# Optimization experiments

Measured on AMD Instinct MI355X. Metric: run time of the kernel, lower is better.

Reference implementation:

```python
import jax, jax.numpy as jnp
import numpy as np

B, IN, O, F, FH = 512, 2000, 64, 8, 32
D = 64 + FH * O  # 2112


def setup_inputs() -> dict:
    key = jax.random.key(0)
    ks = jax.random.split(key, 17)
    rn = lambda k, s: jax.random.normal(k, s, dtype=jnp.float32) * 0.05
    return dict(
        x=rn(ks[0], (B, IN)),
        fc_in_W=rn(ks[1], (1024, IN)), fc_in_b=rn(ks[2], (1024,)),
        fc1_W=rn(ks[3], (128, 1024)), fc1_b=rn(ks[4], (128,)),
        out1_W=rn(ks[5], (O, 64, 128)), out1_b=rn(ks[6], (O, 64)),
        coef_nn_W=rn(ks[7], (F, FH, 1)), coef_nn_b=rn(ks[8], (F, FH)),
        coef_att_W=rn(ks[9], (F, FH, FH)),
        out_att_W=rn(ks[10], (O, FH, FH)),
        nodes_trans_W=rn(ks[11], (O, O)),
        trans_gcn_W=rn(ks[12], (D, D)),
        outmap_W=rn(ks[13], (1, D)), outmap_b=rn(ks[14], (1,)),
        prelu_a=jnp.float32(0.25),
        coef_m=rn(ks[15], (O, O, F)),
    )


def reference(x, fc_in_W, fc_in_b, fc1_W, fc1_b, out1_W, out1_b,
              coef_nn_W, coef_nn_b, coef_att_W, out_att_W,
              nodes_trans_W, trans_gcn_W, outmap_W, outmap_b, prelu_a, coef_m):
    elu = jax.nn.elu
    # trunk MLP
    h = jax.nn.relu(x @ fc_in_W.T + fc_in_b)          # [B,1024]
    h = jax.nn.relu(h @ fc1_W.T + fc1_b)              # [B,128]
    # per-output-node heads (vectorized over the output_dim loop)
    hiddens = jax.nn.relu(jnp.einsum('bk,odk->bod', h, out1_W) + out1_b)  # [B,O,64]
    # per-feature coef embedding: Linear(1,FH) on each coef_m[:,:,i] slice
    cf = elu(coef_m[..., None] * coef_nn_W[:, :, 0] + coef_nn_b)          # [O,O,F,FH]
    # sum over concatenated feature axis (F*FH) of exp(elu(.))
    s = jnp.exp(elu(cf)).sum(axis=(2, 3))[:, :, None, None]               # [O,O,1,1]
    lin = jnp.einsum('xyfh,fgh->xyfg', cf, coef_att_W)                    # per-feature attention linear
    p = elu(jnp.exp(elu(cf)) * lin / s)
    cfs = elu(p.sum(axis=2) / F)                                          # [O,O,FH]
    # node-level attention (vectorized over the output_dim loop)
    coef_sum = jnp.exp(elu(cfs)).sum(axis=1)                              # [O,FH]
    p2 = jnp.exp(elu(cfs)) / coef_sum[:, None, :]                         # [O,O,FH]
    lin2 = jnp.einsum('oih,igh->oig', cfs, out_att_W)
    att = (p2 * lin2).reshape(O, O * FH)                                  # concat over i (i-major)
    hc = jnp.concatenate(
        [hiddens, jnp.broadcast_to(att[None], (x.shape[0], O, O * FH))], axis=2)  # [B,O,D]
    nt = jnp.einsum('bpd,op->bod', hc, nodes_trans_W)                     # node mixing Linear(O,O)
    trans = jax.nn.sigmoid(jnp.einsum('bod,ed->boe', nt, trans_gcn_W))    # [B,O,D]
    z = (trans @ outmap_W.T + outmap_b).squeeze(-1)                       # [B,O]
    return jnp.where(z >= 0, z, prelu_a * z)                              # PReLU
```

## Files before the change

### kernel.cpp

```cpp
#include <hip/hip_runtime.h>
#include <math.h>

typedef __attribute__((ext_vector_type(8))) short bf16x8;
typedef __attribute__((ext_vector_type(4))) float f32x4;

static __device__ __forceinline__ float fast_elu(float x) {
    return x > 0.0f ? x : __expf(x) - 1.0f;
}

static __device__ __forceinline__ unsigned short f2bf(float f) {
    unsigned int u = __float_as_uint(f);
    unsigned int r = (u + 0x7FFFu + ((u >> 16) & 1u)) >> 16;
    return (unsigned short)r;
}

static __device__ __forceinline__ bf16x8 cvt8(const float* __restrict__ s) {
    float4 a = *reinterpret_cast<const float4*>(s);
    float4 b = *reinterpret_cast<const float4*>(s + 4);
    bf16x8 r;
    r[0] = (short)f2bf(a.x); r[1] = (short)f2bf(a.y);
    r[2] = (short)f2bf(a.z); r[3] = (short)f2bf(a.w);
    r[4] = (short)f2bf(b.x); r[5] = (short)f2bf(b.y);
    r[6] = (short)f2bf(b.z); r[7] = (short)f2bf(b.w);
    return r;
}

#define S0 131072
#define S1 393216
#define S2 409600
#define S3 410112
#define S4 475648
#define S5 492544
#define CONV_BLOCKS 1924

static __device__ __forceinline__ void conv_phase(
    int bx,
    const float* __restrict__ x, const float* __restrict__ fcinW,
    const float* __restrict__ fc1W, const float* __restrict__ ntW,
    const float* __restrict__ out1W, const float* __restrict__ tgw,
    unsigned short* __restrict__ xb, unsigned short* __restrict__ fcinWb,
    unsigned short* __restrict__ fc1Wb, unsigned short* __restrict__ Wb,
    unsigned short* __restrict__ out1WbT, unsigned short* __restrict__ Gb)
{
    int u = bx * 256 + threadIdx.x;
    if (u < S0) {
        int r = u >> 8, c = u & 255;
        bf16x8 v;
        if (c < 250) v = cvt8(&x[(size_t)r * 2000 + c * 8]);
        else { bf16x8 z = {0,0,0,0,0,0,0,0}; v = z; }
        *reinterpret_cast<bf16x8*>(&xb[(size_t)r * 2048 + c * 8]) = v;
    } else if (u < S1) {
        int i = u - S0;
        int r = i >> 8, c = i & 255;
        bf16x8 v;
        if (c < 250) v = cvt8(&fcinW[(size_t)r * 2000 + c * 8]);
        else { bf16x8 z = {0,0,0,0,0,0,0,0}; v = z; }
        *reinterpret_cast<bf16x8*>(&fcinWb[(size_t)r * 2048 + c * 8]) = v;
    } else if (u < S2) {
        int i8 = (u - S1) * 8;
        *reinterpret_cast<bf16x8*>(&fc1Wb[i8]) = cvt8(&fc1W[i8]);
    } else if (u < S3) {
        int i8 = (u - S2) * 8;
        *reinterpret_cast<bf16x8*>(&Wb[i8]) = cvt8(&ntW[i8]);
    } else if (u < S4) {
        int i = u - S3;
        int n = i >> 4, kc = i & 15;
        int d = n >> 6, p = n & 63;
        *reinterpret_cast<bf16x8*>(&out1WbT[(size_t)n * 128 + kc * 8]) =
            cvt8(&out1W[(size_t)((p << 6) | d) * 128 + kc * 8]);
    } else if (u < S5) {
        int i = u - S4;
        int e = i >> 3, c = i & 7;
        *reinterpret_cast<bf16x8*>(&Gb[(size_t)e * 64 + c * 8]) =
            cvt8(&tgw[(size_t)e * 2112 + c * 8]);
    }
}

static __device__ __forceinline__ void coef_phase(
    int bx, float* __restrict__ smemf,
    const float* __restrict__ coef_m, const float* __restrict__ cW,
    const float* __restrict__ cB, const float* __restrict__ attW,
    float* __restrict__ cfs)
{
    float* cf_s = smemf;
    float* part = smemf + 1024;
    const int t = threadIdx.x;
    const int wv = t >> 6, lane = t & 63;
    const int xy = bx * 4 + wv;
    float ls = 0.0f;
    #pragma unroll
    for (int i = 0; i < 4; ++i) {
        int idx = i * 64 + lane;
        int f = idx >> 5;
        float v = fast_elu(coef_m[xy * 8 + f] * cW[idx] + cB[idx]);
        cf_s[wv * 256 + idx] = v;
        ls += __expf(fast_elu(v));
    }
    #pragma unroll
    for (int m = 1; m < 64; m <<= 1) ls += __shfl_xor(ls, m, 64);
    __syncthreads();
    const float rs = __builtin_amdgcn_rcpf(ls);
    const int g = lane & 31, fg = lane >> 5;
    float acc = 0.0f;
    for (int f = fg * 4; f < fg * 4 + 4; ++f) {
        float lin = 0.0f;
        #pragma unroll
        for (int h = 0; h < 32; h += 4) {
            float4 Lv = *reinterpret_cast<const float4*>(&cf_s[wv * 256 + f * 32 + h]);
            float4 Wv = *reinterpret_cast<const float4*>(&attW[f * 1024 + g * 32 + h]);
            lin += Lv.x * Wv.x + Lv.y * Wv.y + Lv.z * Wv.z + Lv.w * Wv.w;
        }
        float e = __expf(fast_elu(cf_s[wv * 256 + f * 32 + g]));
        acc += fast_elu(e * lin * rs);
    }
    part[wv * 64 + lane] = acc;
    __syncthreads();
    if (lane < 32) {
        float tot = part[wv * 64 + lane] + part[wv * 64 + lane + 32];
        cfs[xy * 32 + lane] = fast_elu(tot * 0.125f);
    }
}

static __device__ __forceinline__ void att_phase(
    int o, int ic, float* __restrict__ smemf,
    const float* __restrict__ cfs, const float* __restrict__ oattW,
    float* __restrict__ att)
{
    float* L    = smemf;
    float* red  = smemf + 2048;
    float* csum = smemf + 2304;
    const int t = threadIdx.x;
    #pragma unroll
    for (int j = 0; j < 8; ++j) L[t + 256 * j] = cfs[o * 2048 + t + 256 * j];
    __syncthreads();
    {
        int h = t & 31, ig = t >> 5;
        float ps = 0.0f;
        for (int i = ig * 8; i < ig * 8 + 8; ++i) ps += __expf(fast_elu(L[i * 32 + h]));
        red[t] = ps;
        __syncthreads();
        if (t < 32) {
            float cs = 0.0f;
            #pragma unroll
            for (int j = 0; j < 8; ++j) cs += red[j * 32 + t];
            csum[t] = cs;
        }
        __syncthreads();
    }
    int idx = ic * 256 + t;
    int i = idx >> 5, g = idx & 31;
    float lin2 = 0.0f;
    #pragma unroll
    for (int h = 0; h < 32; h += 4) {
        float4 Lv = *reinterpret_cast<const float4*>(&L[i * 32 + h]);
        float4 Wv = *reinterpret_cast<const float4*>(&oattW[i * 1024 + g * 32 + h]);
        lin2 += Lv.x * Wv.x + Lv.y * Wv.y + Lv.z * Wv.z + Lv.w * Wv.w;
    }
    float p2 = __expf(fast_elu(L[idx])) * __builtin_amdgcn_rcpf(csum[g]);
    att[o * 2048 + idx] = p2 * lin2;
}

static __device__ __forceinline__ void natt_phase(
    int bx, float* __restrict__ smemf,
    const float* __restrict__ ntW, const float* __restrict__ att,
    unsigned short* __restrict__ nattb)
{
    float* ntW_s = smemf;
    float* att_s = smemf + 64 * 65;
    const int t = threadIdx.x;
    const int d0 = bx * 16;
    #pragma unroll
    for (int j = 0; j < 16; ++j) {
        int idx = t + 256 * j;
        ntW_s[(idx >> 6) * 65 + (idx & 63)] = ntW[idx];
    }
    #pragma unroll
    for (int j = 0; j < 4; ++j) {
        int idx = t + 256 * j;
        int p = idx >> 4, dd = idx & 15;
        att_s[p * 17 + dd] = att[p * 2048 + d0 + dd];
    }
    __syncthreads();
    const int dd = t & 15, ob = (t >> 4) * 4;
    float acc[4] = {0.0f, 0.0f, 0.0f, 0.0f};
    for (int p = 0; p < 64; ++p) {
        float av = att_s[p * 17 + dd];
        #pragma unroll
        for (int i = 0; i < 4; ++i) acc[i] += ntW_s[(ob + i) * 65 + p] * av;
    }
    #pragma unroll
    for (int i = 0; i < 4; ++i)
        nattb[(ob + i) * 2048 + d0 + dd] = f2bf(acc[i]);
}

static __device__ __forceinline__ void gemm_core(
    const unsigned short* __restrict__ A, int lda,
    const unsigned short* __restrict__ B, int ldb,
    float* __restrict__ C, unsigned short* __restrict__ Cb,
    int ldc, long strideCz, const float* __restrict__ bias,
    int mode, int kchunk, int bn, int bm, int bz,
    unsigned short* __restrict__ As, unsigned short* __restrict__ Bs)
{
    const int t = threadIdx.x;
    const int w = t >> 6, lane = t & 63, l16 = lane & 15, quad = lane >> 4;
    const int n0 = bn * 64, m0 = bm * 64;
    const int kb0 = bz * kchunk;
    const int r = t >> 2, koff = (t & 3) * 8;
    if (mode == 0) C += (size_t)bz * strideCz;

    const size_t arow = (size_t)(m0 + r) * lda + koff;
    const size_t brow = (size_t)(n0 + r) * ldb + koff;
    bf16x8 av = *reinterpret_cast<const bf16x8*>(&A[arow + kb0]);
    bf16x8 bv = *reinterpret_cast<const bf16x8*>(&B[brow + kb0]);

    f32x4 acc[4] = {};
    for (int kb = kb0; kb < kb0 + kchunk; kb += 32) {
        __syncthreads();
        *reinterpret_cast<bf16x8*>(&As[r * 40 + koff]) = av;
        *reinterpret_cast<bf16x8*>(&Bs[r * 40 + koff]) = bv;
        if (kb + 32 < kb0 + kchunk) {
            av = *reinterpret_cast<const bf16x8*>(&A[arow + kb + 32]);
            bv = *reinterpret_cast<const bf16x8*>(&B[brow + kb + 32]);
        }
        __syncthreads();
        bf16x8 af = *reinterpret_cast<const bf16x8*>(&As[(w * 16 + l16) * 40 + quad * 8]);
        #pragma unroll
        for (int nt = 0; nt < 4; ++nt) {
            bf16x8 bf = *reinterpret_cast<const bf16x8*>(&Bs[(nt * 16 + l16) * 40 + quad * 8]);
            acc[nt] = __builtin_amdgcn_mfma_f32_16x16x32_bf16(af, bf, acc[nt], 0, 0, 0);
        }
    }
    #pragma unroll
    for (int nt = 0; nt < 4; ++nt)
        #pragma unroll
        for (int i = 0; i < 4; ++i) {
            int m = m0 + w * 16 + quad * 4 + i;
            int n = n0 + nt * 16 + l16;
            if (mode == 0) {
                C[(size_t)m * ldc + n] = acc[nt][i];
            } else {
                int bidx = (((n & 63) << 6) | (n >> 6));
                float v = acc[nt][i] + bias[bidx];
                v = fmaxf(v, 0.0f);
                Cb[(size_t)m * ldc + n] = f2bf(v);
            }
        }
}

static __device__ __forceinline__ void gemm_tgwa_core(
    const float* __restrict__ tgw,
    const unsigned short* __restrict__ B,
    float* __restrict__ C, long strideCz,
    int kchunk, int bm, int bz,
    unsigned short* __restrict__ As, unsigned short* __restrict__ Bs)
{
    const int t = threadIdx.x;
    const int w = t >> 6, lane = t & 63, l16 = lane & 15, quad = lane >> 4;
    const int m0 = bm * 64;
    const int kb0 = bz * kchunk;
    const int r = t >> 2, koff = (t & 3) * 8;
    C += (size_t)bz * strideCz;

    const float* arow = tgw + (size_t)(m0 + r) * 2112 + 64 + koff;
    const unsigned short* brow = B + (size_t)r * 2048 + koff;
    bf16x8 av = cvt8(arow + kb0);
    bf16x8 bv = *reinterpret_cast<const bf16x8*>(brow + kb0);

    f32x4 acc[4] = {};
    for (int kb = kb0; kb < kb0 + kchunk; kb += 32) {
        __syncthreads();
        *reinterpret_cast<bf16x8*>(&As[r * 40 + koff]) = av;
        *reinterpret_cast<bf16x8*>(&Bs[r * 40 + koff]) = bv;
        if (kb + 32 < kb0 + kchunk) {
            av = cvt8(arow + kb + 32);
            bv = *reinterpret_cast<const bf16x8*>(brow + kb + 32);
        }
        __syncthreads();
        bf16x8 af = *reinterpret_cast<const bf16x8*>(&As[(w * 16 + l16) * 40 + quad * 8]);
        #pragma unroll
        for (int nt = 0; nt < 4; ++nt) {
            bf16x8 bf = *reinterpret_cast<const bf16x8*>(&Bs[(nt * 16 + l16) * 40 + quad * 8]);
            acc[nt] = __builtin_amdgcn_mfma_f32_16x16x32_bf16(af, bf, acc[nt], 0, 0, 0);
        }
    }
    #pragma unroll
    for (int nt = 0; nt < 4; ++nt)
        #pragma unroll
        for (int i = 0; i < 4; ++i) {
            int m = m0 + w * 16 + quad * 4 + i;
            int n = nt * 16 + l16;
            C[(size_t)m * 64 + n] = acc[nt][i];
        }
}

static __device__ __forceinline__ void gemm_fa_core(
    const float* __restrict__ Ap, int lda, long apstride, int nparts,
    const float* __restrict__ abias,
    const unsigned short* __restrict__ B, int ldb,
    float* __restrict__ C, unsigned short* __restrict__ Cb,
    int ldc, long strideCz, const float* __restrict__ bias,
    int mode, int kchunk, int bn, int bm, int bz,
    unsigned short* __restrict__ As, unsigned short* __restrict__ Bs)
{
    const int t = threadIdx.x;
    const int w = t >> 6, lane = t & 63, l16 = lane & 15, quad = lane >> 4;
    const int n0 = bn * 64, m0 = bm * 64;
    const int kb0 = bz * kchunk;
    const int r = t >> 2, koff = (t & 3) * 8;
    if (mode == 0) C += (size_t)bz * strideCz;

    f32x4 acc[4] = {};
    for (int kb = kb0; kb < kb0 + kchunk; kb += 32) {
        float a8[8];
        {
            const float* base = &Ap[(size_t)(m0 + r) * lda + kb + koff];
            float4 s0 = *reinterpret_cast<const float4*>(base);
            float4 s1 = *reinterpret_cast<const float4*>(base + 4);
            for (int j = 1; j < nparts; ++j) {
                const float* pj = base + (size_t)j * apstride;
                float4 p0 = *reinterpret_cast<const float4*>(pj);
                float4 p1 = *reinterpret_cast<const float4*>(pj + 4);
                s0.x += p0.x; s0.y += p0.y; s0.z += p0.z; s0.w += p0.w;
                s1.x += p1.x; s1.y += p1.y; s1.z += p1.z; s1.w += p1.w;
            }
            float4 b0 = *reinterpret_cast<const float4*>(&abias[kb + koff]);
            float4 b1 = *reinterpret_cast<const float4*>(&abias[kb + koff + 4]);
            a8[0] = fmaxf(s0.x + b0.x, 0.0f); a8[1] = fmaxf(s0.y + b0.y, 0.0f);
            a8[2] = fmaxf(s0.z + b0.z, 0.0f); a8[3] = fmaxf(s0.w + b0.w, 0.0f);
            a8[4] = fmaxf(s1.x + b1.x, 0.0f); a8[5] = fmaxf(s1.y + b1.y, 0.0f);
            a8[6] = fmaxf(s1.z + b1.z, 0.0f); a8[7] = fmaxf(s1.w + b1.w, 0.0f);
        }
        bf16x8 bv = *reinterpret_cast<const bf16x8*>(&B[(size_t)(n0 + r) * ldb + kb + koff]);
        __syncthreads();
        ushort4 lo, hi;
        lo.x = f2bf(a8[0]); lo.y = f2bf(a8[1]); lo.z = f2bf(a8[2]); lo.w = f2bf(a8[3]);
        hi.x = f2bf(a8[4]); hi.y = f2bf(a8[5]); hi.z = f2bf(a8[6]); hi.w = f2bf(a8[7]);
        *reinterpret_cast<ushort4*>(&As[r * 40 + koff]) = lo;
        *reinterpret_cast<ushort4*>(&As[r * 40 + koff + 4]) = hi;
        *reinterpret_cast<bf16x8*>(&Bs[r * 40 + koff]) = bv;
        __syncthreads();
        bf16x8 af = *reinterpret_cast<const bf16x8*>(&As[(w * 16 + l16) * 40 + quad * 8]);
        #pragma unroll
        for (int nt = 0; nt < 4; ++nt) {
            bf16x8 bf = *reinterpret_cast<const bf16x8*>(&Bs[(nt * 16 + l16) * 40 + quad * 8]);
            acc[nt] = __builtin_amdgcn_mfma_f32_16x16x32_bf16(af, bf, acc[nt], 0, 0, 0);
        }
    }
    #pragma unroll
    for (int nt = 0; nt < 4; ++nt)
        #pragma unroll
        for (int i = 0; i < 4; ++i) {
            int m = m0 + w * 16 + quad * 4 + i;
            int n = n0 + nt * 16 + l16;
            if (mode == 0) {
                C[(size_t)m * ldc + n] = acc[nt][i];
            } else {
                int bidx = (((n & 63) << 6) | (n >> 6));
                float v = acc[nt][i] + bias[bidx];
                v = fmaxf(v, 0.0f);
                Cb[(size_t)m * ldc + n] = f2bf(v);
            }
        }
}

static __device__ __forceinline__ void nt1f_phase(
    int b, unsigned short* __restrict__ smemu,
    const unsigned short* __restrict__ hbT, const unsigned short* __restrict__ Wb,
    unsigned short* __restrict__ nt1b)
{
    unsigned short* HtT   = smemu;
    unsigned short* nt1_s = smemu + 64 * 72;
    const int t = threadIdx.x;
    const int w = t >> 6, lane = t & 63, l16 = lane & 15, quad = lane >> 4;

    const unsigned short* src = hbT + (size_t)b * 4096;
    #pragma unroll
    for (int j = 0; j < 2; ++j) {
        int c = t + j * 256;
        *reinterpret_cast<bf16x8*>(&HtT[(c >> 3) * 72 + (c & 7) * 8]) =
            *reinterpret_cast<const bf16x8*>(&src[c * 8]);
    }
    __syncthreads();

    bf16x8 aW[2];
    #pragma unroll
    for (int h = 0; h < 2; ++h)
        aW[h] = *reinterpret_cast<const bf16x8*>(&Wb[(w * 16 + l16) * 64 + h * 32 + quad * 8]);
    #pragma unroll
    for (int dt = 0; dt < 4; ++dt) {
        f32x4 acc = {0.0f, 0.0f, 0.0f, 0.0f};
        #pragma unroll
        for (int h = 0; h < 2; ++h) {
            bf16x8 bf = *reinterpret_cast<const bf16x8*>(
                &HtT[(dt * 16 + l16) * 72 + h * 32 + quad * 8]);
            acc = __builtin_amdgcn_mfma_f32_16x16x32_bf16(aW[h], bf, acc, 0, 0, 0);
        }
        #pragma unroll
        for (int i = 0; i < 4; ++i)
            nt1_s[(w * 16 + quad * 4 + i) * 72 + dt * 16 + l16] = f2bf(acc[i]);
    }
    __syncthreads();
    #pragma unroll
    for (int j = 0; j < 2; ++j) {
        int c = t + j * 256;
        *reinterpret_cast<bf16x8*>(&nt1b[(size_t)b * 4096 + c * 8]) =
            *reinterpret_cast<const bf16x8*>(&nt1_s[(c >> 3) * 72 + (c & 7) * 8]);
    }
}

__global__ __launch_bounds__(256) void uber1(
    const float* x, const float* fcinW, const float* fc1W, const float* ntW,
    const float* out1W, const float* tgw,
    unsigned short* xb, unsigned short* fcinWb, unsigned short* fc1Wb,
    unsigned short* Wb, unsigned short* out1WbT, unsigned short* Gb,
    const float* coef_m, const float* cW, const float* cB, const float* attW,
    float* cfs)
{
    __shared__ __align__(16) float smemf[1280];
    int bx = blockIdx.x;
    if (bx < CONV_BLOCKS)
        conv_phase(bx, x, fcinW, fc1W, ntW, out1W, tgw,
                   xb, fcinWb, fc1Wb, Wb, out1WbT, Gb);
    else
        coef_phase(bx - CONV_BLOCKS, smemf, coef_m, cW, cB, attW, cfs);
}

__global__ __launch_bounds__(256) void uber2(
    const unsigned short* xb, const unsigned short* fcinWb, float* h1p,
    const float* cfs, const float* oattW, float* att)
{
    __shared__ __align__(16) float smemf[2592];
    int bx = blockIdx.x;
    if (bx < 1024) {
        unsigned short* As = (unsigned short*)smemf;
        gemm_core(xb, 2048, fcinWb, 2048, h1p, nullptr, 1024, 524288L,
                  nullptr, 0, 256, bx & 15, (bx >> 4) & 7, bx >> 7, As, As + 2560);
    } else {
        int b2 = bx - 1024;
        att_phase(b2 & 63, b2 >> 6, smemf, cfs, oattW, att);
    }
}

__global__ __launch_bounds__(256) void uber3(
    const float* h1p, const float* fc_in_b, const unsigned short* fc1Wb,
    float* h2p,
    const float* ntW, const float* att, unsigned short* nattb)
{
    __shared__ __align__(16) float smemf[5248];
    int bx = blockIdx.x;
    if (bx < 64) {
        unsigned short* As = (unsigned short*)smemf;
        gemm_fa_core(h1p, 1024, 524288L, 8, fc_in_b, fc1Wb, 1024,
                     h2p, nullptr, 128, 65536L, nullptr, 0, 256,
                     bx & 1, (bx >> 1) & 7, bx >> 4, As, As + 2560);
    } else {
        natt_phase(bx - 64, smemf, ntW, att, nattb);
    }
}

__global__ __launch_bounds__(256) void uber4(
    const float* h2p, const float* fc1_b, const unsigned short* out1WbT,
    unsigned short* hbT, const float* out1_b,
    const float* tgw, const unsigned short* nattb, float* cpT)
{
    __shared__ __align__(16) float smemf[2560];
    unsigned short* As = (unsigned short*)smemf;
    int bx = blockIdx.x;
    if (bx < 512) {
        gemm_fa_core(h2p, 128, 65536L, 4, fc1_b, out1WbT, 128,
                     nullptr, hbT, 4096, 0L, out1_b, 2, 128,
                     bx & 63, bx >> 6, 0, As, As + 2560);
    } else {
        int b2 = bx - 512;
        gemm_tgwa_core(tgw, nattb, cpT, 135168L, 128,
                       b2 % 33, b2 / 33, As, As + 2560);
    }
}

__global__ __launch_bounds__(256) void uber5(
    const unsigned short* hbT, const unsigned short* Wb, unsigned short* nt1b,
    const float* cpT, float* cmatT)
{
    __shared__ __align__(16) unsigned short smemu[2 * 64 * 72];
    int bx = blockIdx.x;
    if (bx < 512) {
        nt1f_phase(bx, smemu, hbT, Wb, nt1b);
    } else {
        int i = (bx - 512) * 256 + threadIdx.x;
        float a = 0.0f;
        #pragma unroll
        for (int j = 0; j < 16; ++j) a += cpT[i + (long)j * 135168L];
        cmatT[i] = a;
    }
}

__global__ __launch_bounds__(256) void final_eblk(
    const unsigned short* __restrict__ nt1b,
    const unsigned short* __restrict__ Gb,
    const float* __restrict__ cmatT,
    const float* __restrict__ outW,
    float* __restrict__ zpart)
{
    __shared__ __align__(16) unsigned short nls[2][64 * 72];
    __shared__ float zs[2][4][64];
    const int t = threadIdx.x;
    const int w = t >> 6, lane = t & 63, l16 = lane & 15, quad = lane >> 4;
    const int eb = blockIdx.x;
    const int b0 = blockIdx.y * 16;
    const int ew = eb * 64 + w * 16;

    bf16x8 ga[2];
    #pragma unroll
    for (int h = 0; h < 2; ++h)
        ga[h] = *reinterpret_cast<const bf16x8*>(
            &Gb[(size_t)(ew + l16) * 64 + h * 32 + quad * 8]);
    float cm[4][4];
    #pragma unroll
    for (int nt = 0; nt < 4; ++nt)
        #pragma unroll
        for (int i = 0; i < 4; ++i)
            cm[nt][i] = cmatT[(size_t)(ew + quad * 4 + i) * 64 + nt * 16 + l16];
    float wv[4];
    #pragma unroll
    for (int i = 0; i < 4; ++i) wv[i] = outW[ew + quad * 4 + i];

    const int c0 = t, c1 = t + 256;
    bf16x8 v0 = *reinterpret_cast<const bf16x8*>(&nt1b[(size_t)b0 * 4096 + c0 * 8]);
    bf16x8 v1 = *reinterpret_cast<const bf16x8*>(&nt1b[(size_t)b0 * 4096 + c1 * 8]);
    *reinterpret_cast<bf16x8*>(&nls[0][(c0 >> 3) * 72 + (c0 & 7) * 8]) = v0;
    *reinterpret_cast<bf16x8*>(&nls[0][(c1 >> 3) * 72 + (c1 & 7) * 8]) = v1;
    __syncthreads();

    int cur = 0;
    for (int bi = 0; bi < 16; ++bi) {
        if (bi < 15) {
            v0 = *reinterpret_cast<const bf16x8*>(
                &nt1b[(size_t)(b0 + bi + 1) * 4096 + c0 * 8]);
            v1 = *reinterpret_cast<const bf16x8*>(
                &nt1b[(size_t)(b0 + bi + 1) * 4096 + c1 * 8]);
        }
        if (bi > 0 && t < 64) {
            const float* z = &zs[(bi - 1) & 1][0][0];
            zpart[((size_t)eb * 512 + b0 + bi - 1) * 64 + t] =
                z[t] + z[64 + t] + z[128 + t] + z[192 + t];
        }
        float zo[4] = {0.0f, 0.0f, 0.0f, 0.0f};
        #pragma unroll
        for (int nt = 0; nt < 4; ++nt) {
            bf16x8 bf0 = *reinterpret_cast<const bf16x8*>(
                &nls[cur][(nt * 16 + l16) * 72 + quad * 8]);
            bf16x8 bf1 = *reinterpret_cast<const bf16x8*>(
                &nls[cur][(nt * 16 + l16) * 72 + 32 + quad * 8]);
            f32x4 acc = {cm[nt][0], cm[nt][1], cm[nt][2], cm[nt][3]};
            acc = __builtin_amdgcn_mfma_f32_16x16x32_bf16(ga[0], bf0, acc, 0, 0, 0);
            acc = __builtin_amdgcn_mfma_f32_16x16x32_bf16(ga[1], bf1, acc, 0, 0, 0);
            #pragma unroll
            for (int i = 0; i < 4; ++i)
                zo[nt] += __builtin_amdgcn_rcpf(1.0f + __expf(-acc[i])) * wv[i];
        }
        #pragma unroll
        for (int nt = 0; nt < 4; ++nt) {
            zo[nt] += __shfl_xor(zo[nt], 16, 64);
            zo[nt] += __shfl_xor(zo[nt], 32, 64);
        }
        if (quad == 0) {
            #pragma unroll
            for (int nt = 0; nt < 4; ++nt)
                zs[bi & 1][w][nt * 16 + l16] = zo[nt];
        }
        if (bi < 15) {
            *reinterpret_cast<bf16x8*>(&nls[1 - cur][(c0 >> 3) * 72 + (c0 & 7) * 8]) = v0;
            *reinterpret_cast<bf16x8*>(&nls[1 - cur][(c1 >> 3) * 72 + (c1 & 7) * 8]) = v1;
        }
        __syncthreads();
        cur ^= 1;
    }
    if (t < 64) {
        const float* z = &zs[1][0][0];
        zpart[((size_t)eb * 512 + b0 + 15) * 64 + t] =
            z[t] + z[64 + t] + z[128 + t] + z[192 + t];
    }
}

__global__ __launch_bounds__(256) void finish_kernel(
    const float* __restrict__ zpart, const float* __restrict__ outB,
    const float* __restrict__ preluA, float* __restrict__ out)
{
    int i = blockIdx.x * 256 + threadIdx.x;
    float z = 0.0f;
    for (int j = 0; j < 33; ++j) z += zpart[(size_t)j * 32768 + i];
    z += outB[0];
    float pa = preluA[0];
    out[i] = (z >= 0.0f) ? z : pa * z;
}

extern "C" void kernel_launch(void* const* d_in, const int* in_sizes, int n_in,
                              void* d_out, int out_size, void* d_ws, size_t ws_size,
                              hipStream_t stream)
{
    const float* x       = (const float*)d_in[0];
    const float* fc_in_W = (const float*)d_in[1];
    const float* fc_in_b = (const float*)d_in[2];
    const float* fc1_W   = (const float*)d_in[3];
    const float* fc1_b   = (const float*)d_in[4];
    const float* out1_W  = (const float*)d_in[5];
    const float* out1_b  = (const float*)d_in[6];
    const float* cW      = (const float*)d_in[7];
    const float* cB      = (const float*)d_in[8];
    const float* cattW   = (const float*)d_in[9];
    const float* oattW   = (const float*)d_in[10];
    const float* ntW     = (const float*)d_in[11];
    const float* tgw     = (const float*)d_in[12];
    const float* outW    = (const float*)d_in[13];
    const float* outB    = (const float*)d_in[14];
    const float* preluA  = (const float*)d_in[15];
    const float* coef_m  = (const float*)d_in[16];
    float* out = (float*)d_out;
    float* ws  = (float*)d_ws;

    unsigned short* xb      = (unsigned short*)(ws + 0);
    unsigned short* fcinWb  = (unsigned short*)(ws + 524288);
    unsigned short* fc1Wb   = (unsigned short*)(ws + 1572864);
    unsigned short* Wb      = (unsigned short*)(ws + 1638400);
    unsigned short* out1WbT = (unsigned short*)(ws + 1640448);
    unsigned short* Gb      = (unsigned short*)(ws + 1902592);
    float*          cfs     = ws + 1970176;
    float*          att     = ws + 2101248;
    unsigned short* nattb   = (unsigned short*)(ws + 2232320);
    float*          h1p     = ws + 2297856;
    float*          h2p     = ws + 6492160;
    unsigned short* hbT     = (unsigned short*)(ws + 6754304);
    float*          cpT     = ws + 7802880;
    float*          cmatT   = ws + 9965568;
    unsigned short* nt1b    = (unsigned short*)(ws + 10100736);
    float*          zpart   = ws + 11149312;

    uber1<<<CONV_BLOCKS + 1024, 256, 0, stream>>>(
        x, fc_in_W, fc1_W, ntW, out1_W, tgw,
        xb, fcinWb, fc1Wb, Wb, out1WbT, Gb,
        coef_m, cW, cB, cattW, cfs);
    uber2<<<1536, 256, 0, stream>>>(xb, fcinWb, h1p, cfs, oattW, att);
    uber3<<<192, 256, 0, stream>>>(h1p, fc_in_b, fc1Wb, h2p, ntW, att, nattb);
    uber4<<<1040, 256, 0, stream>>>(h2p, fc1_b, out1WbT, hbT, out1_b,
                                    tgw, nattb, cpT);
    uber5<<<1040, 256, 0, stream>>>(hbT, Wb, nt1b, cpT, cmatT);
    final_eblk<<<dim3(33, 32), 256, 0, stream>>>(nt1b, Gb, cmatT, outW, zpart);
    finish_kernel<<<128, 256, 0, stream>>>(zpart, outB, preluA, out);
}
```

Measured before the change: 198.2 us.

## Halve split-K partitions and rewrite final kernel without shared memory staging

The fc_in GEMM split-K chunk grows from 256 to 512, which halves the partial buffers and the blocks. The downstream reduction now sums 4 partials instead of 8, and the tgw GEMM K-chunk doubles so cmat reduces 8 partials instead of 16. The final kernel is rewritten so each warp holds all four e-tiles of G in registers and loads its nt1b fragment straight from global memory. This removes the LDS double buffer, the barriers and the cross-warp z reduction. The trade-off is fewer blocks for parallelism and more registers per thread.

```diff
diff --git a/kernel.cpp b/kernel.cpp
--- a/kernel.cpp
+++ b/kernel.cpp
@@ -431,12 +431,12 @@
 {
     __shared__ __align__(16) float smemf[2592];
     int bx = blockIdx.x;
-    if (bx < 1024) {
+    if (bx < 512) {
         unsigned short* As = (unsigned short*)smemf;
         gemm_core(xb, 2048, fcinWb, 2048, h1p, nullptr, 1024, 524288L,
-                  nullptr, 0, 256, bx & 15, (bx >> 4) & 7, bx >> 7, As, As + 2560);
+                  nullptr, 0, 512, bx & 15, (bx >> 4) & 7, bx >> 7, As, As + 2560);
     } else {
-        int b2 = bx - 1024;
+        int b2 = bx - 512;
         att_phase(b2 & 63, b2 >> 6, smemf, cfs, oattW, att);
     }
 }
@@ -450,7 +450,7 @@
     int bx = blockIdx.x;
     if (bx < 64) {
         unsigned short* As = (unsigned short*)smemf;
-        gemm_fa_core(h1p, 1024, 524288L, 8, fc_in_b, fc1Wb, 1024,
+        gemm_fa_core(h1p, 1024, 524288L, 4, fc_in_b, fc1Wb, 1024,
                      h2p, nullptr, 128, 65536L, nullptr, 0, 256,
                      bx & 1, (bx >> 1) & 7, bx >> 4, As, As + 2560);
     } else {
@@ -472,7 +472,7 @@
                      bx & 63, bx >> 6, 0, As, As + 2560);
     } else {
         int b2 = bx - 512;
-        gemm_tgwa_core(tgw, nattb, cpT, 135168L, 128,
+        gemm_tgwa_core(tgw, nattb, cpT, 135168L, 256,
                        b2 % 33, b2 / 33, As, As + 2560);
     }
 }
@@ -487,98 +487,69 @@
         nt1f_phase(bx, smemu, hbT, Wb, nt1b);
     } else {
         int i = (bx - 512) * 256 + threadIdx.x;
-        float a = 0.0f;
-        #pragma unroll
-        for (int j = 0; j < 16; ++j) a += cpT[i + (long)j * 135168L];
-        cmatT[i] = a;
-    }
-}
-
-__global__ __launch_bounds__(256) void final_eblk(
+        if (i < 135168) {
+            float a = 0.0f;
+            #pragma unroll
+            for (int j = 0; j < 8; ++j) a += cpT[i + (long)j * 135168L];
+            cmatT[i] = a;
+        }
+    }
+}
+
+__global__ __launch_bounds__(256) void final_nb(
     const unsigned short* __restrict__ nt1b,
     const unsigned short* __restrict__ Gb,
     const float* __restrict__ cmatT,
     const float* __restrict__ outW,
     float* __restrict__ zpart)
 {
-    __shared__ __align__(16) unsigned short nls[2][64 * 72];
-    __shared__ float zs[2][4][64];
     const int t = threadIdx.x;
     const int w = t >> 6, lane = t & 63, l16 = lane & 15, quad = lane >> 4;
     const int eb = blockIdx.x;
     const int b0 = blockIdx.y * 16;
-    const int ew = eb * 64 + w * 16;
-
-    bf16x8 ga[2];
-    #pragma unroll
-    for (int h = 0; h < 2; ++h)
-        ga[h] = *reinterpret_cast<const bf16x8*>(
-            &Gb[(size_t)(ew + l16) * 64 + h * 32 + quad * 8]);
-    float cm[4][4];
-    #pragma unroll
-    for (int nt = 0; nt < 4; ++nt)
-        #pragma unroll
-        for (int i = 0; i < 4; ++i)
-            cm[nt][i] = cmatT[(size_t)(ew + quad * 4 + i) * 64 + nt * 16 + l16];
-    float wv[4];
-    #pragma unroll
-    for (int i = 0; i < 4; ++i) wv[i] = outW[ew + quad * 4 + i];
-
-    const int c0 = t, c1 = t + 256;
-    bf16x8 v0 = *reinterpret_cast<const bf16x8*>(&nt1b[(size_t)b0 * 4096 + c0 * 8]);
-    bf16x8 v1 = *reinterpret_cast<const bf16x8*>(&nt1b[(size_t)b0 * 4096 + c1 * 8]);
-    *reinterpret_cast<bf16x8*>(&nls[0][(c0 >> 3) * 72 + (c0 & 7) * 8]) = v0;
-    *reinterpret_cast<bf16x8*>(&nls[0][(c1 >> 3) * 72 + (c1 & 7) * 8]) = v1;
-    __syncthreads();
-
-    int cur = 0;
+    const int o = w * 16 + l16;
+
+    bf16x8 ga[4][2];
+    float cm[4][4], wv[4][4];
+    #pragma unroll
+    for (int et = 0; et < 4; ++et) {
+        #pragma unroll
+        for (int h = 0; h < 2; ++h)
+            ga[et][h] = *reinterpret_cast<const bf16x8*>(
+                &Gb[(size_t)(eb * 64 + et * 16 + l16) * 64 + h * 32 + quad * 8]);
+        #pragma unroll
+        for (int i = 0; i < 4; ++i) {
+            int e = eb * 64 + et * 16 + quad * 4 + i;
+            cm[et][i] = cmatT[(size_t)e * 64 + o];
+            wv[et][i] = outW[e];
+        }
+    }
+
+    const unsigned short* bbase = nt1b + (size_t)b0 * 4096 + o * 64 + quad * 8;
+    bf16x8 bf0 = *reinterpret_cast<const bf16x8*>(bbase);
+    bf16x8 bf1 = *reinterpret_cast<const bf16x8*>(bbase + 32);
+
     for (int bi = 0; bi < 16; ++bi) {
+        bf16x8 nb0, nb1;
         if (bi < 15) {
-            v0 = *reinterpret_cast<const bf16x8*>(
-                &nt1b[(size_t)(b0 + bi + 1) * 4096 + c0 * 8]);
-            v1 = *reinterpret_cast<const bf16x8*>(
-                &nt1b[(size_t)(b0 + bi + 1) * 4096 + c1 * 8]);
-        }
-        if (bi > 0 && t < 64) {
-            const float* z = &zs[(bi - 1) & 1][0][0];
-            zpart[((size_t)eb * 512 + b0 + bi - 1) * 64 + t] =
-                z[t] + z[64 + t] + z[128 + t] + z[192 + t];
-        }
-        float zo[4] = {0.0f, 0.0f, 0.0f, 0.0f};
-        #pragma unroll
-        for (int nt = 0; nt < 4; ++nt) {
-            bf16x8 bf0 = *reinterpret_cast<const bf16x8*>(
-                &nls[cur][(nt * 16 + l16) * 72 + quad * 8]);
-            bf16x8 bf1 = *reinterpret_cast<const bf16x8*>(
-                &nls[cur][(nt * 16 + l16) * 72 + 32 + quad * 8]);
-            f32x4 acc = {cm[nt][0], cm[nt][1], cm[nt][2], cm[nt][3]};
-            acc = __builtin_amdgcn_mfma_f32_16x16x32_bf16(ga[0], bf0, acc, 0, 0, 0);
-            acc = __builtin_amdgcn_mfma_f32_16x16x32_bf16(ga[1], bf1, acc, 0, 0, 0);
+            nb0 = *reinterpret_cast<const bf16x8*>(bbase + (size_t)(bi + 1) * 4096);
+            nb1 = *reinterpret_cast<const bf16x8*>(bbase + (size_t)(bi + 1) * 4096 + 32);
+        }
+        float zo = 0.0f;
+        #pragma unroll
+        for (int et = 0; et < 4; ++et) {
+            f32x4 acc = {cm[et][0], cm[et][1], cm[et][2], cm[et][3]};
+            acc = __builtin_amdgcn_mfma_f32_16x16x32_bf16(ga[et][0], bf0, acc, 0, 0, 0);
+            acc = __builtin_amdgcn_mfma_f32_16x16x32_bf16(ga[et][1], bf1, acc, 0, 0, 0);
             #pragma unroll
             for (int i = 0; i < 4; ++i)
-                zo[nt] += __builtin_amdgcn_rcpf(1.0f + __expf(-acc[i])) * wv[i];
-        }
-        #pragma unroll
-        for (int nt = 0; nt < 4; ++nt) {
-            zo[nt] += __shfl_xor(zo[nt], 16, 64);
-            zo[nt] += __shfl_xor(zo[nt], 32, 64);
-        }
-        if (quad == 0) {
-            #pragma unroll
-            for (int nt = 0; nt < 4; ++nt)
-                zs[bi & 1][w][nt * 16 + l16] = zo[nt];
-        }
-        if (bi < 15) {
-            *reinterpret_cast<bf16x8*>(&nls[1 - cur][(c0 >> 3) * 72 + (c0 & 7) * 8]) = v0;
-            *reinterpret_cast<bf16x8*>(&nls[1 - cur][(c1 >> 3) * 72 + (c1 & 7) * 8]) = v1;
-        }
-        __syncthreads();
-        cur ^= 1;
-    }
-    if (t < 64) {
-        const float* z = &zs[1][0][0];
-        zpart[((size_t)eb * 512 + b0 + 15) * 64 + t] =
-            z[t] + z[64 + t] + z[128 + t] + z[192 + t];
+                zo += __builtin_amdgcn_rcpf(1.0f + __expf(-acc[i])) * wv[et][i];
+        }
+        zo += __shfl_xor(zo, 16, 64);
+        zo += __shfl_xor(zo, 32, 64);
+        if (quad == 0)
+            zpart[((size_t)eb * 512 + b0 + bi) * 64 + o] = zo;
+        bf0 = nb0; bf1 = nb1;
     }
 }
 
@@ -628,22 +599,22 @@
     float*          att     = ws + 2101248;
     unsigned short* nattb   = (unsigned short*)(ws + 2232320);
     float*          h1p     = ws + 2297856;
-    float*          h2p     = ws + 6492160;
-    unsigned short* hbT     = (unsigned short*)(ws + 6754304);
-    float*          cpT     = ws + 7802880;
-    float*          cmatT   = ws + 9965568;
-    unsigned short* nt1b    = (unsigned short*)(ws + 10100736);
-    float*          zpart   = ws + 11149312;
+    float*          h2p     = ws + 4395008;
+    unsigned short* hbT     = (unsigned short*)(ws + 4657152);
+    float*          cpT     = ws + 5705728;
+    float*          cmatT   = ws + 6787072;
+    unsigned short* nt1b    = (unsigned short*)(ws + 6922240);
+    float*          zpart   = ws + 7970816;
 
     uber1<<<CONV_BLOCKS + 1024, 256, 0, stream>>>(
         x, fc_in_W, fc1_W, ntW, out1_W, tgw,
         xb, fcinWb, fc1Wb, Wb, out1WbT, Gb,
         coef_m, cW, cB, cattW, cfs);
-    uber2<<<1536, 256, 0, stream>>>(xb, fcinWb, h1p, cfs, oattW, att);
+    uber2<<<1024, 256, 0, stream>>>(xb, fcinWb, h1p, cfs, oattW, att);
     uber3<<<192, 256, 0, stream>>>(h1p, fc_in_b, fc1Wb, h2p, ntW, att, nattb);
-    uber4<<<1040, 256, 0, stream>>>(h2p, fc1_b, out1WbT, hbT, out1_b,
-                                    tgw, nattb, cpT);
+    uber4<<<776, 256, 0, stream>>>(h2p, fc1_b, out1WbT, hbT, out1_b,
+                                   tgw, nattb, cpT);
     uber5<<<1040, 256, 0, stream>>>(hbT, Wb, nt1b, cpT, cmatT);
-    final_eblk<<<dim3(33, 32), 256, 0, stream>>>(nt1b, Gb, cmatT, outW, zpart);
+    final_nb<<<dim3(33, 32), 256, 0, stream>>>(nt1b, Gb, cmatT, outW, zpart);
     finish_kernel<<<128, 256, 0, stream>>>(zpart, outB, preluA, out);
 }
```

After: 193.9 us. -2.2%, faster.
